# Optimization experiments

Hardware: AMD Instinct MI355X
Metric: run time of the kernel (lower is better)

The kernel has to match this reference:

```python
import jax, jax.numpy as jnp
from jax import lax
import numpy as np

B, H, W = 16, 512, 512
NBINS = 256
MARGIN_EYE = 12
BLUR_SIZE = 5
ALPHA_SKIN, ALPHA_EYE, ALPHA_LIP = 0.3, 0.8, 0.1


def de_norm(x):
    return jnp.clip((x + 1.0) * 0.5, 0.0, 1.0)


def renorm(x):
    return x * 2.0 - 1.0


def _match_channel(src, ref, w_s, w_r):
    # src/ref: (P,) pixel values in [0,255]; w_s/w_r: (P,) mask weights
    b_s = jnp.clip(src.astype(jnp.int32), 0, NBINS - 1)
    b_r = jnp.clip(ref.astype(jnp.int32), 0, NBINS - 1)
    h_s = jnp.zeros((NBINS,), src.dtype).at[b_s].add(w_s)   # masked histogram
    h_r = jnp.zeros((NBINS,), ref.dtype).at[b_r].add(w_r)
    cdf_s = jnp.cumsum(h_s) / jnp.maximum(jnp.sum(h_s), 1e-6)
    cdf_r = jnp.cumsum(h_r) / jnp.maximum(jnp.sum(h_r), 1e-6)
    # CDF-matching transfer table (equiv. of cal_trans in PSGAN/EleGANt)
    table = jnp.clip(jnp.searchsorted(cdf_r, cdf_s), 0, NBINS - 1).astype(src.dtype)
    return table[b_s]


def masked_his_match(image_s, image_r, mask_s, mask_r):
    # image: (3,H,W), mask: (1,H,W)
    s = de_norm(image_s) * 255.0 * mask_s
    r = de_norm(image_r) * 255.0 * mask_r
    w_s = mask_s.reshape(-1)
    w_r = mask_r.reshape(-1)
    matched = jax.vmap(_match_channel, in_axes=(0, 0, None, None))(
        s.reshape(3, -1), r.reshape(3, -1), w_s, w_r).reshape(s.shape)
    matched = jnp.where(mask_s > 0, matched, s)  # only masked pixels replaced
    return renorm(matched / 255.0)


def expand_area(mask, margin):
    # morphological dilation (max pool) of (1,H,W) mask
    k = 2 * margin + 1
    return lax.reduce_window(mask, 0.0, lax.max, (1, k, k), (1, 1, 1), 'SAME')


def mask_blur(mask, blur_size):
    # box blur; 'valid' mode: blurred support kept inside original mask
    k = blur_size
    s = lax.reduce_window(mask, 0.0, lax.add, (1, k, k), (1, 1, 1), 'SAME') / float(k * k)
    return s * mask


def generate_pgt(image_s, image_r, mask_s, mask_r, lms_s, lms_r):
    pgt = image_s
    # skin (channel 1)
    m = mask_s[1:2]
    pgt = (1.0 - m) * pgt + m * masked_his_match(image_s, image_r, m, mask_r[1:2])
    # neck (channel 4)
    m = mask_s[4:5]
    pgt = (1.0 - m) * pgt + m * masked_his_match(image_s, image_r, m, mask_r[4:5])
    # lip (channel 0)
    m = mask_s[0:1]
    pgt = (1.0 - m) * pgt + m * masked_his_match(image_s, image_r, m, mask_r[0:1])
    # eyes (channels 2,3), dilated and intersected with skin
    m_se = expand_area(jnp.sum(mask_s[2:4], axis=0, keepdims=True), MARGIN_EYE) * mask_s[1:2]
    m_re = expand_area(jnp.sum(mask_r[2:4], axis=0, keepdims=True), MARGIN_EYE) * mask_r[1:2]
    eye_match = masked_his_match(image_s, image_r, m_se, m_re)
    mb = mask_blur(m_se, BLUR_SIZE)
    pgt = (1.0 - mb) * pgt + mb * eye_match
    # fine_align (reconstructed, simplified: per-region alpha blend of reference,
    # landmark warp omitted -- helper source not provided)
    for m, a in ((mask_s[1:2], ALPHA_SKIN), (m_se, ALPHA_EYE), (mask_s[0:1], ALPHA_LIP)):
        pgt = (1.0 - a * m) * pgt + (a * m) * image_r
    return pgt


def setup_inputs() -> dict:
    key = jax.random.key(0)
    ks = jax.random.split(key, 6)
    sources = jax.random.uniform(ks[0], (B, 3, H, W), jnp.float32, -1.0, 1.0)
    targets = jax.random.uniform(ks[1], (B, 3, H, W), jnp.float32, -1.0, 1.0)
    mask_srcs = (jax.random.uniform(ks[2], (B, 5, H, W)) < 0.3).astype(jnp.float32)
    mask_tars = (jax.random.uniform(ks[3], (B, 5, H, W)) < 0.3).astype(jnp.float32)
    lms_srcs = jax.random.uniform(ks[4], (B, 68, 2), jnp.float32, 0.0, float(H))
    lms_tars = jax.random.uniform(ks[5], (B, 68, 2), jnp.float32, 0.0, float(H))
    return {"sources": sources, "targets": targets, "mask_srcs": mask_srcs,
            "mask_tars": mask_tars, "lms_srcs": lms_srcs, "lms_tars": lms_tars}


def reference(sources, targets, mask_srcs, mask_tars, lms_srcs, lms_tars):
    # vmap over batch replaces the per-sample Python loop of ComposePGT.forward
    return jax.vmap(generate_pgt)(sources, targets, mask_srcs, mask_tars, lms_srcs, lms_tars)
```

## Files before the change

### kernel.cpp

```cpp
#include <hip/hip_runtime.h>
#include <stdint.h>

#define BB 16
#define HH 512
#define WW 512
#define HW (HH*WW)
#define NB 256


__device__ __forceinline__ float denorm255(float x) {
    return fminf(fmaxf((x + 1.0f) * 0.5f, 0.0f), 1.0f) * 255.0f;
}
__device__ __forceinline__ float renorm_lut(int t) {
    return ((float)t / 255.0f) * 2.0f - 1.0f;
}
__device__ __forceinline__ uint32_t alignb(uint32_t hi, uint32_t lo, int r) {
    return (uint32_t)(((((uint64_t)hi) << 32) | lo) >> (8 * r));
}

__global__ void __launch_bounds__(256) prep_kernel(
    const float* __restrict__ ms, const float* __restrict__ mr,
    uint32_t* __restrict__ C)
{
    int t = blockIdx.x * 256 + threadIdx.x;
    const int perSide = BB * (HW / 4);
    int side = t / perSide;
    int rem  = t - side * perSide;
    int b    = rem / (HW / 4);
    int c    = rem - b * (HW / 4);
    const float* base = (side == 0 ? ms : mr) + (size_t)b * 5 * HW;
    float4 m0 = ((const float4*)(base + 0 * (size_t)HW))[c];
    float4 m1 = ((const float4*)(base + 1 * (size_t)HW))[c];
    float4 m2 = ((const float4*)(base + 2 * (size_t)HW))[c];
    float4 m3 = ((const float4*)(base + 3 * (size_t)HW))[c];
    float4 m4 = ((const float4*)(base + 4 * (size_t)HW))[c];
    float a0[4] = {m0.x, m0.y, m0.z, m0.w};
    float a1[4] = {m1.x, m1.y, m1.z, m1.w};
    float a2[4] = {m2.x, m2.y, m2.z, m2.w};
    float a3[4] = {m3.x, m3.y, m3.z, m3.w};
    float a4[4] = {m4.x, m4.y, m4.z, m4.w};
    uint32_t w = 0;
    #pragma unroll
    for (int j = 0; j < 4; j++) {
        uint32_t e  = (uint32_t)(a2[j] + a3[j]);
        uint32_t pb = (a0[j] > 0.f ? 4u : 0u) | (a1[j] > 0.f ? 8u : 0u)
                    | (a4[j] > 0.f ? 16u : 0u);
        w |= (e | pb) << (8 * j);
    }
    C[t] = w;
}

__global__ void __launch_bounds__(256) hor_kernel(
    const uint32_t* __restrict__ C, uint32_t* __restrict__ eh)
{
    int t   = blockIdx.x * 256 + threadIdx.x;
    int row = t >> 7;
    int w   = t & 127;
    const uint32_t* rp = C + (size_t)row * 128;
    uint32_t arr[7];
    #pragma unroll
    for (int k = 0; k < 7; k++) {
        int idx = w + k - 3;
        arr[k] = (idx >= 0 && idx < 128) ? (rp[idx] & 0x03030303u) : 0u;
    }
    uint32_t acc = arr[3];
    #pragma unroll
    for (int s = 1; s <= 12; s++) {
        int a = s >> 2, r = s & 3;
        uint32_t vp, vm;
        if (r == 0) {
            vp = arr[3 + a];
            vm = arr[3 - a];
        } else {
            vp = alignb(arr[3 + a + 1], arr[3 + a], r);
            int am = (s + 3) >> 2;
            vm = alignb(arr[3 - am + 1], arr[3 - am], 4 - r);
        }
        acc |= vp | vm;
    }
    eh[t] = acc;
}

__global__ void __launch_bounds__(256) ver_kernel(
    const uint32_t* __restrict__ eh, uint32_t* __restrict__ C)
{
    int t   = blockIdx.x * 256 + threadIdx.x;
    int sb  = t >> 12;
    int rem = t & 4095;
    int yg  = rem >> 5;
    int ck  = rem & 31;
    int y0  = yg << 2;
    const uint4* P = (const uint4*)(eh + (size_t)sb * (HW / 4));
    auto R = [&](int y) -> uint4 {
        uint4 z = {0, 0, 0, 0};
        if (y < 0 || y >= HH) return z;
        return P[y * 32 + ck];
    };
    uint4 core = {0, 0, 0, 0};
    #pragma unroll
    for (int yy = -9; yy <= 12; yy++) {
        uint4 r = R(y0 + yy);
        core.x |= r.x; core.y |= r.y; core.z |= r.z; core.w |= r.w;
    }
    uint4 b0 = R(y0 - 12), b1 = R(y0 - 11), b2 = R(y0 - 10);
    uint4 a0 = R(y0 + 13), a1 = R(y0 + 14), a2 = R(y0 + 15);

    uint4* C4 = (uint4*)(C + (size_t)sb * (HW / 4));
    #pragma unroll
    for (int i = 0; i < 4; i++) {
        uint4 v = core;
        if (i == 0) { v.x|=b0.x|b1.x|b2.x; v.y|=b0.y|b1.y|b2.y; v.z|=b0.z|b1.z|b2.z; v.w|=b0.w|b1.w|b2.w; }
        if (i == 1) { v.x|=b1.x|b2.x|a0.x; v.y|=b1.y|b2.y|a0.y; v.z|=b1.z|b2.z|a0.z; v.w|=b1.w|b2.w|a0.w; }
        if (i == 2) { v.x|=b2.x|a0.x|a1.x; v.y|=b2.y|a0.y|a1.y; v.z|=b2.z|a0.z|a1.z; v.w|=b2.w|a0.w|a1.w; }
        if (i == 3) { v.x|=a0.x|a1.x|a2.x; v.y|=a0.y|a1.y|a2.y; v.z|=a0.z|a1.z|a2.z; v.w|=a0.w|a1.w|a2.w; }
        int idx = (y0 + i) * 32 + ck;
        uint4 cw = C4[idx];
        #pragma unroll
        for (int q = 0; q < 4; q++) {
            uint32_t vv = (&v.x)[q];
            uint32_t cc = (&cw.x)[q];
            uint32_t t3 = vv & (vv >> 1) & 0x01010101u;
            vv -= t3;
            uint32_t m1b = (cc >> 3) & 0x01010101u;
            vv &= m1b * 255u;
            (&cw.x)[q] = cc | (vv << 5);
        }
        C4[idx] = cw;
    }
}

__global__ void __launch_bounds__(256) blur_kernel(
    const uint32_t* __restrict__ C, uint32_t* __restrict__ mbs)
{
    int t   = blockIdx.x * 256 + threadIdx.x;
    int b   = t >> 14;
    b = t >> 16;
    int rem = t & 65535;
    int y   = rem >> 7;
    int w   = rem & 127;
    const uint32_t* P = C + (size_t)b * (HW / 4);
    uint32_t vm1 = 0, v0 = 0, vp1 = 0;
    #pragma unroll
    for (int dy = -2; dy <= 2; dy++) {
        int yy = y + dy;
        if (yy < 0 || yy >= HH) continue;
        const uint32_t* rp = P + yy * 128;
        if (w > 0)   vm1 += (rp[w - 1] >> 5) & 0x03030303u;
        v0 += (rp[w] >> 5) & 0x03030303u;
        if (w < 127) vp1 += (rp[w + 1] >> 5) & 0x03030303u;
    }
    uint32_t s = v0;
    s += alignb(v0, vm1, 2);
    s += alignb(v0, vm1, 3);
    s += alignb(vp1, v0, 1);
    s += alignb(vp1, v0, 2);
    mbs[t] = s;
}

#define HB 64
__global__ void __launch_bounds__(256) hist_kernel(
    const float* __restrict__ src, const float* __restrict__ tgt,
    const uint32_t* __restrict__ C, int* __restrict__ hist)
{
    int bs  = blockIdx.x / HB;
    int blk = blockIdx.x % HB;
    int b = bs >> 1, side = bs & 1;
    const float* img = (side ? tgt : src) + (size_t)b * 3 * HW;
    const float4* i0 = (const float4*)(img);
    const float4* i1 = (const float4*)(img + HW);
    const float4* i2 = (const float4*)(img + 2 * (size_t)HW);
    const uint32_t* pc = C + (size_t)(side * BB + b) * (HW / 4);

    __shared__ int h[12 * NB];
    for (int i = threadIdx.x; i < 12 * NB; i += 256) h[i] = 0;
    __syncthreads();

    for (int c = blk * 256 + threadIdx.x; c < HW / 4; c += HB * 256) {
        float4 v0 = i0[c], v1 = i1[c], v2 = i2[c];
        uint32_t cw = pc[c];
        float d0[4] = {denorm255(v0.x), denorm255(v0.y), denorm255(v0.z), denorm255(v0.w)};
        float d1[4] = {denorm255(v1.x), denorm255(v1.y), denorm255(v1.z), denorm255(v1.w)};
        float d2[4] = {denorm255(v2.x), denorm255(v2.y), denorm255(v2.z), denorm255(v2.w)};
        #pragma unroll
        for (int j = 0; j < 4; j++) {
            uint32_t pb = (cw >> (8 * j)) & 0xFFu;
            if (pb & 8u) {
                atomicAdd(&h[0 * NB + min((int)d0[j], 255)], 1);
                atomicAdd(&h[1 * NB + min((int)d1[j], 255)], 1);
                atomicAdd(&h[2 * NB + min((int)d2[j], 255)], 1);
            }
            if (pb & 16u) {
                atomicAdd(&h[3 * NB + min((int)d0[j], 255)], 1);
                atomicAdd(&h[4 * NB + min((int)d1[j], 255)], 1);
                atomicAdd(&h[5 * NB + min((int)d2[j], 255)], 1);
            }
            if (pb & 4u) {
                atomicAdd(&h[6 * NB + min((int)d0[j], 255)], 1);
                atomicAdd(&h[7 * NB + min((int)d1[j], 255)], 1);
                atomicAdd(&h[8 * NB + min((int)d2[j], 255)], 1);
            }
            int mei = (int)((pb >> 5) & 3u);
            if (mei) {
                float fm = (float)mei;
                atomicAdd(&h[ 9 * NB + min((int)(d0[j] * fm), 255)], mei);
                atomicAdd(&h[10 * NB + min((int)(d1[j] * fm), 255)], mei);
                atomicAdd(&h[11 * NB + min((int)(d2[j] * fm), 255)], mei);
            }
        }
    }
    __syncthreads();
    int* gh = hist + (size_t)bs * 12 * NB;
    for (int i = threadIdx.x; i < 12 * NB; i += 256)
        if (h[i]) atomicAdd(&gh[i], h[i]);
}

__global__ void __launch_bounds__(NB) table_kernel(
    const int* __restrict__ hist, uint8_t* __restrict__ table)
{
    int idx = blockIdx.x;
    int c = idx % 3; int rest = idx / 3; int rg = rest & 3; int b = rest >> 2;
    const int* hs = hist + ((size_t)((b * 2 + 0) * 4 + rg) * 3 + c) * NB;
    const int* hr = hist + ((size_t)((b * 2 + 1) * 4 + rg) * 3 + c) * NB;
    __shared__ int a[NB];
    __shared__ float cr[NB];
    int t = threadIdx.x;

    a[t] = hs[t];
    __syncthreads();
    for (int off = 1; off < NB; off <<= 1) {
        int v = (t >= off) ? a[t - off] : 0;
        __syncthreads();
        a[t] += v;
        __syncthreads();
    }
    int totS = a[NB - 1];
    int cumS = a[t];
    __syncthreads();

    a[t] = hr[t];
    __syncthreads();
    for (int off = 1; off < NB; off <<= 1) {
        int v = (t >= off) ? a[t - off] : 0;
        __syncthreads();
        a[t] += v;
        __syncthreads();
    }
    int totR = a[NB - 1];
    cr[t] = (float)a[t] / fmaxf((float)totR, 1e-6f);
    float v = (float)cumS / fmaxf((float)totS, 1e-6f);
    __syncthreads();

    int cnt = 0;
    for (int j = 0; j < NB; j++) cnt += (cr[j] < v) ? 1 : 0;
    table[(size_t)idx * NB + t] = (uint8_t)min(cnt, 255);
}

#define CB 64
__global__ void __launch_bounds__(256) compose_kernel(
    const float* __restrict__ src, const float* __restrict__ tgt,
    const uint32_t* __restrict__ C, const uint32_t* __restrict__ mbs,
    const uint8_t* __restrict__ table, float* __restrict__ out)
{
    int b   = blockIdx.x / CB;
    int blk = blockIdx.x % CB;
    __shared__ uint8_t tb[12 * NB];
    const uint8_t* gt = table + (size_t)b * 12 * NB;
    for (int i = threadIdx.x; i < 12 * NB; i += 256) tb[i] = gt[i];
    __syncthreads();

    const float4* s0 = (const float4*)(src + (size_t)b * 3 * HW);
    const float4* s1 = s0 + HW / 4;
    const float4* s2 = s1 + HW / 4;
    const float4* t0 = (const float4*)(tgt + (size_t)b * 3 * HW);
    const float4* t1 = t0 + HW / 4;
    const float4* t2 = t1 + HW / 4;
    const uint32_t* pc = C + (size_t)b * (HW / 4);
    const uint32_t* qc = mbs + (size_t)b * (HW / 4);
    float4* o0 = (float4*)(out + (size_t)b * 3 * HW);
    float4* o1 = o0 + HW / 4;
    float4* o2 = o1 + HW / 4;

    for (int c = blk * 256 + threadIdx.x; c < HW / 4; c += CB * 256) {
        float4 x0 = s0[c], x1 = s1[c], x2 = s2[c];
        float4 r0 = t0[c], r1 = t1[c], r2 = t2[c];
        uint32_t cw = pc[c];
        uint32_t qw = qc[c];
        float X0[4] = {x0.x, x0.y, x0.z, x0.w};
        float X1[4] = {x1.x, x1.y, x1.z, x1.w};
        float X2[4] = {x2.x, x2.y, x2.z, x2.w};
        float R0[4] = {r0.x, r0.y, r0.z, r0.w};
        float R1[4] = {r1.x, r1.y, r1.z, r1.w};
        float R2[4] = {r2.x, r2.y, r2.z, r2.w};
        float O0[4], O1[4], O2[4];
        #pragma unroll
        for (int j = 0; j < 4; j++) {
            uint32_t pb = (cw >> (8 * j)) & 0xFFu;
            float q = (float)((qw >> (8 * j)) & 0xFFu);
            float m0f = (float)((pb >> 2) & 1u);
            float m1f = (float)((pb >> 3) & 1u);
            float m4f = (float)((pb >> 4) & 1u);
            float fm  = (float)((pb >> 5) & 3u);
            float d0 = denorm255(X0[j]), d1 = denorm255(X1[j]), d2 = denorm255(X2[j]);
            float p0 = X0[j], p1 = X1[j], p2 = X2[j];
            {
                float e0 = renorm_lut(tb[0 * NB + min((int)(d0 * m1f), 255)]);
                float e1 = renorm_lut(tb[1 * NB + min((int)(d1 * m1f), 255)]);
                float e2 = renorm_lut(tb[2 * NB + min((int)(d2 * m1f), 255)]);
                p0 = (1.0f - m1f) * p0 + m1f * e0;
                p1 = (1.0f - m1f) * p1 + m1f * e1;
                p2 = (1.0f - m1f) * p2 + m1f * e2;
            }
            {
                float e0 = renorm_lut(tb[3 * NB + min((int)(d0 * m4f), 255)]);
                float e1 = renorm_lut(tb[4 * NB + min((int)(d1 * m4f), 255)]);
                float e2 = renorm_lut(tb[5 * NB + min((int)(d2 * m4f), 255)]);
                p0 = (1.0f - m4f) * p0 + m4f * e0;
                p1 = (1.0f - m4f) * p1 + m4f * e1;
                p2 = (1.0f - m4f) * p2 + m4f * e2;
            }
            {
                float e0 = renorm_lut(tb[6 * NB + min((int)(d0 * m0f), 255)]);
                float e1 = renorm_lut(tb[7 * NB + min((int)(d1 * m0f), 255)]);
                float e2 = renorm_lut(tb[8 * NB + min((int)(d2 * m0f), 255)]);
                p0 = (1.0f - m0f) * p0 + m0f * e0;
                p1 = (1.0f - m0f) * p1 + m0f * e1;
                p2 = (1.0f - m0f) * p2 + m0f * e2;
            }
            {
                float mb = (q * (1.0f / 25.0f)) * fm;
                float e0 = renorm_lut(tb[ 9 * NB + min((int)(d0 * fm), 255)]);
                float e1 = renorm_lut(tb[10 * NB + min((int)(d1 * fm), 255)]);
                float e2 = renorm_lut(tb[11 * NB + min((int)(d2 * fm), 255)]);
                p0 = (1.0f - mb) * p0 + mb * e0;
                p1 = (1.0f - mb) * p1 + mb * e1;
                p2 = (1.0f - mb) * p2 + mb * e2;
            }
            float a = 0.3f * m1f;
            p0 = (1.0f - a) * p0 + a * R0[j];
            p1 = (1.0f - a) * p1 + a * R1[j];
            p2 = (1.0f - a) * p2 + a * R2[j];
            a = 0.8f * fm;
            p0 = (1.0f - a) * p0 + a * R0[j];
            p1 = (1.0f - a) * p1 + a * R1[j];
            p2 = (1.0f - a) * p2 + a * R2[j];
            a = 0.1f * m0f;
            p0 = (1.0f - a) * p0 + a * R0[j];
            p1 = (1.0f - a) * p1 + a * R1[j];
            p2 = (1.0f - a) * p2 + a * R2[j];
            O0[j] = p0; O1[j] = p1; O2[j] = p2;
        }
        float4 w0 = {O0[0], O0[1], O0[2], O0[3]};
        float4 w1 = {O1[0], O1[1], O1[2], O1[3]};
        float4 w2 = {O2[0], O2[1], O2[2], O2[3]};
        o0[c] = w0; o1[c] = w1; o2[c] = w2;
    }
}

extern "C" void kernel_launch(void* const* d_in, const int* in_sizes, int n_in,
                              void* d_out, int out_size, void* d_ws, size_t ws_size,
                              hipStream_t stream) {
    const float* src = (const float*)d_in[0];
    const float* tgt = (const float*)d_in[1];
    const float* ms  = (const float*)d_in[2];
    const float* mr  = (const float*)d_in[3];
    float* out = (float*)d_out;

    uint8_t* ws = (uint8_t*)d_ws;
    uint32_t* C   = (uint32_t*)(ws);
    uint32_t* eh  = (uint32_t*)(ws + (size_t)2 * BB * HW);
    uint32_t* mbs = (uint32_t*)(ws + (size_t)4 * BB * HW);
    int* hist     = (int*)(ws + (size_t)5 * BB * HW);
    uint8_t* table = ws + (size_t)5 * BB * HW + (size_t)2 * BB * 12 * NB * 4;

    hipMemsetAsync(hist, 0, (size_t)2 * BB * 12 * NB * sizeof(int), stream);

    prep_kernel<<<2 * BB * HW / 4 / 256, 256, 0, stream>>>(ms, mr, C);
    hor_kernel<<<2 * BB * HW / 4 / 256, 256, 0, stream>>>(C, eh);
    ver_kernel<<<2 * BB * (HH / 4) * (WW / 16) / 256, 256, 0, stream>>>(eh, C);
    blur_kernel<<<BB * HW / 4 / 256, 256, 0, stream>>>(C, mbs);
    hist_kernel<<<2 * BB * HB, 256, 0, stream>>>(src, tgt, C, hist);
    table_kernel<<<BB * 4 * 3, NB, 0, stream>>>(hist, table);
    compose_kernel<<<BB * CB, 256, 0, stream>>>(src, tgt, C, mbs, table, out);
}
```

Baseline: 343.1 us.

## Fuse mask prep with horizontal dilation and widen per-thread work in blur, hist, compose

Mask packing and horizontal dilation now run in one kernel that shares the row through LDS, so the intermediate packed mask is no longer re-read from global memory by a separate pass. Blur now handles 16 pixels per thread with uint4 loads. The histogram kernel processes 8 pixels per iteration with half as many blocks. Compose drops its grid-stride loop for one thread per 8 pixels, which means many more blocks each reloading the 3 KB LUT into shared memory. That extra per-block LUT load is the main added cost.

```diff
diff --git a/kernel.cpp b/kernel.cpp
--- a/kernel.cpp
+++ b/kernel.cpp
@@ -18,67 +18,85 @@
     return (uint32_t)(((((uint64_t)hi) << 32) | lo) >> (8 * r));
 }
 
-__global__ void __launch_bounds__(256) prep_kernel(
+__global__ void __launch_bounds__(256) prep_hor_kernel(
     const float* __restrict__ ms, const float* __restrict__ mr,
-    uint32_t* __restrict__ C)
-{
-    int t = blockIdx.x * 256 + threadIdx.x;
-    const int perSide = BB * (HW / 4);
-    int side = t / perSide;
-    int rem  = t - side * perSide;
-    int b    = rem / (HW / 4);
-    int c    = rem - b * (HW / 4);
-    const float* base = (side == 0 ? ms : mr) + (size_t)b * 5 * HW;
-    float4 m0 = ((const float4*)(base + 0 * (size_t)HW))[c];
-    float4 m1 = ((const float4*)(base + 1 * (size_t)HW))[c];
-    float4 m2 = ((const float4*)(base + 2 * (size_t)HW))[c];
-    float4 m3 = ((const float4*)(base + 3 * (size_t)HW))[c];
-    float4 m4 = ((const float4*)(base + 4 * (size_t)HW))[c];
-    float a0[4] = {m0.x, m0.y, m0.z, m0.w};
-    float a1[4] = {m1.x, m1.y, m1.z, m1.w};
-    float a2[4] = {m2.x, m2.y, m2.z, m2.w};
-    float a3[4] = {m3.x, m3.y, m3.z, m3.w};
-    float a4[4] = {m4.x, m4.y, m4.z, m4.w};
-    uint32_t w = 0;
-    #pragma unroll
-    for (int j = 0; j < 4; j++) {
-        uint32_t e  = (uint32_t)(a2[j] + a3[j]);
-        uint32_t pb = (a0[j] > 0.f ? 4u : 0u) | (a1[j] > 0.f ? 8u : 0u)
-                    | (a4[j] > 0.f ? 16u : 0u);
-        w |= (e | pb) << (8 * j);
-    }
-    C[t] = w;
-}
-
-__global__ void __launch_bounds__(256) hor_kernel(
-    const uint32_t* __restrict__ C, uint32_t* __restrict__ eh)
-{
-    int t   = blockIdx.x * 256 + threadIdx.x;
-    int row = t >> 7;
-    int w   = t & 127;
-    const uint32_t* rp = C + (size_t)row * 128;
-    uint32_t arr[7];
-    #pragma unroll
-    for (int k = 0; k < 7; k++) {
-        int idx = w + k - 3;
-        arr[k] = (idx >= 0 && idx < 128) ? (rp[idx] & 0x03030303u) : 0u;
-    }
-    uint32_t acc = arr[3];
-    #pragma unroll
-    for (int s = 1; s <= 12; s++) {
-        int a = s >> 2, r = s & 3;
-        uint32_t vp, vm;
-        if (r == 0) {
-            vp = arr[3 + a];
-            vm = arr[3 - a];
-        } else {
-            vp = alignb(arr[3 + a + 1], arr[3 + a], r);
-            int am = (s + 3) >> 2;
-            vm = alignb(arr[3 - am + 1], arr[3 - am], 4 - r);
-        }
-        acc |= vp | vm;
-    }
-    eh[t] = acc;
+    uint4* __restrict__ C, uint4* __restrict__ eh)
+{
+    int blk  = blockIdx.x;
+    int side = blk >> 10;
+    int rem  = blk & 1023;
+    int b    = rem >> 6;
+    int rg   = rem & 63;
+    int r    = threadIdx.x >> 5;
+    int c    = threadIdx.x & 31;
+    int y    = (rg << 3) + r;
+
+    const float* base = (side ? mr : ms) + (size_t)b * 5 * HW + (size_t)y * WW + c * 16;
+
+    float4 v[5][4];
+    #pragma unroll
+    for (int p = 0; p < 5; p++) {
+        const float4* pp = (const float4*)(base + (size_t)p * HW);
+        #pragma unroll
+        for (int q = 0; q < 4; q++) v[p][q] = pp[q];
+    }
+    uint4 cw, ew;
+    #pragma unroll
+    for (int w = 0; w < 4; w++) {
+        uint32_t wc = 0;
+        #pragma unroll
+        for (int j = 0; j < 4; j++) {
+            float a0 = (&v[0][w].x)[j];
+            float a1 = (&v[1][w].x)[j];
+            float a2 = (&v[2][w].x)[j];
+            float a3 = (&v[3][w].x)[j];
+            float a4 = (&v[4][w].x)[j];
+            uint32_t e  = (uint32_t)(a2 + a3);
+            uint32_t pb = (a0 > 0.f ? 4u : 0u) | (a1 > 0.f ? 8u : 0u)
+                        | (a4 > 0.f ? 16u : 0u);
+            wc |= (e | pb) << (8 * j);
+        }
+        (&cw.x)[w] = wc;
+        (&ew.x)[w] = wc & 0x03030303u;
+    }
+    size_t plane = (size_t)(side * BB + b);
+    int widx = y * 32 + c;
+    C[plane * (HW / 16) + widx] = cw;
+
+    __shared__ uint4 se[8][32];
+    se[r][c] = ew;
+    __syncthreads();
+
+    const uint4 zero4 = {0u, 0u, 0u, 0u};
+    uint4 L = (c > 0)  ? se[r][c - 1] : zero4;
+    uint4 M = se[r][c];
+    uint4 R = (c < 31) ? se[r][c + 1] : zero4;
+    uint32_t W[12] = {L.x, L.y, L.z, L.w, M.x, M.y, M.z, M.w, R.x, R.y, R.z, R.w};
+
+    uint4 outw;
+    #pragma unroll
+    for (int k = 0; k < 4; k++) {
+        uint32_t arr[7];
+        #pragma unroll
+        for (int i = 0; i < 7; i++) arr[i] = W[k + 1 + i];
+        uint32_t acc = arr[3];
+        #pragma unroll
+        for (int s = 1; s <= 12; s++) {
+            int a = s >> 2, rr = s & 3;
+            uint32_t vp, vm;
+            if (rr == 0) {
+                vp = arr[3 + a];
+                vm = arr[3 - a];
+            } else {
+                vp = alignb(arr[3 + a + 1], arr[3 + a], rr);
+                int am = (s + 3) >> 2;
+                vm = alignb(arr[3 - am + 1], arr[3 - am], 4 - rr);
+            }
+            acc |= vp | vm;
+        }
+        (&outw.x)[k] = acc;
+    }
+    eh[plane * (HW / 16) + widx] = outw;
 }
 
 __global__ void __launch_bounds__(256) ver_kernel(
@@ -130,34 +148,79 @@
 }
 
 __global__ void __launch_bounds__(256) blur_kernel(
-    const uint32_t* __restrict__ C, uint32_t* __restrict__ mbs)
-{
-    int t   = blockIdx.x * 256 + threadIdx.x;
-    int b   = t >> 14;
-    b = t >> 16;
-    int rem = t & 65535;
-    int y   = rem >> 7;
-    int w   = rem & 127;
+    const uint32_t* __restrict__ C, uint4* __restrict__ mbs)
+{
+    int t = blockIdx.x * 256 + threadIdx.x;
+    int b = t >> 14;
+    int rem = t & 16383;
+    int y = rem >> 5;
+    int c = rem & 31;
     const uint32_t* P = C + (size_t)b * (HW / 4);
-    uint32_t vm1 = 0, v0 = 0, vp1 = 0;
+    int c4 = c << 2;
+    uint32_t s[6] = {0u, 0u, 0u, 0u, 0u, 0u};
     #pragma unroll
     for (int dy = -2; dy <= 2; dy++) {
         int yy = y + dy;
         if (yy < 0 || yy >= HH) continue;
         const uint32_t* rp = P + yy * 128;
-        if (w > 0)   vm1 += (rp[w - 1] >> 5) & 0x03030303u;
-        v0 += (rp[w] >> 5) & 0x03030303u;
-        if (w < 127) vp1 += (rp[w + 1] >> 5) & 0x03030303u;
-    }
-    uint32_t s = v0;
-    s += alignb(v0, vm1, 2);
-    s += alignb(v0, vm1, 3);
-    s += alignb(vp1, v0, 1);
-    s += alignb(vp1, v0, 2);
-    mbs[t] = s;
-}
-
-#define HB 64
+        uint32_t l = (c > 0)  ? rp[c4 - 1] : 0u;
+        uint4 m = *((const uint4*)(rp + c4));
+        uint32_t rr = (c < 31) ? rp[c4 + 4] : 0u;
+        s[0] += (l   >> 5) & 0x03030303u;
+        s[1] += (m.x >> 5) & 0x03030303u;
+        s[2] += (m.y >> 5) & 0x03030303u;
+        s[3] += (m.z >> 5) & 0x03030303u;
+        s[4] += (m.w >> 5) & 0x03030303u;
+        s[5] += (rr  >> 5) & 0x03030303u;
+    }
+    uint4 o;
+    #pragma unroll
+    for (int k = 0; k < 4; k++) {
+        uint32_t v = s[k + 1];
+        v += alignb(s[k + 1], s[k],     2);
+        v += alignb(s[k + 1], s[k],     3);
+        v += alignb(s[k + 2], s[k + 1], 1);
+        v += alignb(s[k + 2], s[k + 1], 2);
+        (&o.x)[k] = v;
+    }
+    mbs[t] = o;
+}
+
+#define HB 32
+__device__ __forceinline__ void hist4(int* h, uint32_t cw,
+                                      float4 v0, float4 v1, float4 v2)
+{
+    float d0[4] = {denorm255(v0.x), denorm255(v0.y), denorm255(v0.z), denorm255(v0.w)};
+    float d1[4] = {denorm255(v1.x), denorm255(v1.y), denorm255(v1.z), denorm255(v1.w)};
+    float d2[4] = {denorm255(v2.x), denorm255(v2.y), denorm255(v2.z), denorm255(v2.w)};
+    #pragma unroll
+    for (int j = 0; j < 4; j++) {
+        uint32_t pb = (cw >> (8 * j)) & 0xFFu;
+        if (pb & 8u) {
+            atomicAdd(&h[0 * NB + min((int)d0[j], 255)], 1);
+            atomicAdd(&h[1 * NB + min((int)d1[j], 255)], 1);
+            atomicAdd(&h[2 * NB + min((int)d2[j], 255)], 1);
+        }
+        if (pb & 16u) {
+            atomicAdd(&h[3 * NB + min((int)d0[j], 255)], 1);
+            atomicAdd(&h[4 * NB + min((int)d1[j], 255)], 1);
+            atomicAdd(&h[5 * NB + min((int)d2[j], 255)], 1);
+        }
+        if (pb & 4u) {
+            atomicAdd(&h[6 * NB + min((int)d0[j], 255)], 1);
+            atomicAdd(&h[7 * NB + min((int)d1[j], 255)], 1);
+            atomicAdd(&h[8 * NB + min((int)d2[j], 255)], 1);
+        }
+        int mei = (int)((pb >> 5) & 3u);
+        if (mei) {
+            float fm = (float)mei;
+            atomicAdd(&h[ 9 * NB + min((int)(d0[j] * fm), 255)], mei);
+            atomicAdd(&h[10 * NB + min((int)(d1[j] * fm), 255)], mei);
+            atomicAdd(&h[11 * NB + min((int)(d2[j] * fm), 255)], mei);
+        }
+    }
+}
+
 __global__ void __launch_bounds__(256) hist_kernel(
     const float* __restrict__ src, const float* __restrict__ tgt,
     const uint32_t* __restrict__ C, int* __restrict__ hist)
@@ -169,44 +232,19 @@
     const float4* i0 = (const float4*)(img);
     const float4* i1 = (const float4*)(img + HW);
     const float4* i2 = (const float4*)(img + 2 * (size_t)HW);
-    const uint32_t* pc = C + (size_t)(side * BB + b) * (HW / 4);
+    const uint2* pc = (const uint2*)(C + (size_t)(side * BB + b) * (HW / 4));
 
     __shared__ int h[12 * NB];
     for (int i = threadIdx.x; i < 12 * NB; i += 256) h[i] = 0;
     __syncthreads();
 
-    for (int c = blk * 256 + threadIdx.x; c < HW / 4; c += HB * 256) {
-        float4 v0 = i0[c], v1 = i1[c], v2 = i2[c];
-        uint32_t cw = pc[c];
-        float d0[4] = {denorm255(v0.x), denorm255(v0.y), denorm255(v0.z), denorm255(v0.w)};
-        float d1[4] = {denorm255(v1.x), denorm255(v1.y), denorm255(v1.z), denorm255(v1.w)};
-        float d2[4] = {denorm255(v2.x), denorm255(v2.y), denorm255(v2.z), denorm255(v2.w)};
-        #pragma unroll
-        for (int j = 0; j < 4; j++) {
-            uint32_t pb = (cw >> (8 * j)) & 0xFFu;
-            if (pb & 8u) {
-                atomicAdd(&h[0 * NB + min((int)d0[j], 255)], 1);
-                atomicAdd(&h[1 * NB + min((int)d1[j], 255)], 1);
-                atomicAdd(&h[2 * NB + min((int)d2[j], 255)], 1);
-            }
-            if (pb & 16u) {
-                atomicAdd(&h[3 * NB + min((int)d0[j], 255)], 1);
-                atomicAdd(&h[4 * NB + min((int)d1[j], 255)], 1);
-                atomicAdd(&h[5 * NB + min((int)d2[j], 255)], 1);
-            }
-            if (pb & 4u) {
-                atomicAdd(&h[6 * NB + min((int)d0[j], 255)], 1);
-                atomicAdd(&h[7 * NB + min((int)d1[j], 255)], 1);
-                atomicAdd(&h[8 * NB + min((int)d2[j], 255)], 1);
-            }
-            int mei = (int)((pb >> 5) & 3u);
-            if (mei) {
-                float fm = (float)mei;
-                atomicAdd(&h[ 9 * NB + min((int)(d0[j] * fm), 255)], mei);
-                atomicAdd(&h[10 * NB + min((int)(d1[j] * fm), 255)], mei);
-                atomicAdd(&h[11 * NB + min((int)(d2[j] * fm), 255)], mei);
-            }
-        }
+    for (int c = blk * 256 + threadIdx.x; c < HW / 8; c += HB * 256) {
+        uint2 cw = pc[c];
+        float4 a0 = i0[2 * c], b0 = i0[2 * c + 1];
+        float4 a1 = i1[2 * c], b1 = i1[2 * c + 1];
+        float4 a2 = i2[2 * c], b2 = i2[2 * c + 1];
+        hist4(h, cw.x, a0, a1, a2);
+        hist4(h, cw.y, b0, b1, b2);
     }
     __syncthreads();
     int* gh = hist + (size_t)bs * 12 * NB;
@@ -255,17 +293,90 @@
     table[(size_t)idx * NB + t] = (uint8_t)min(cnt, 255);
 }
 
-#define CB 64
+__device__ __forceinline__ void proc4(uint32_t cw, uint32_t qw,
+    float4 x0, float4 x1, float4 x2, float4 r0, float4 r1, float4 r2,
+    const uint8_t* tb, float4& o0, float4& o1, float4& o2)
+{
+    float X0[4] = {x0.x, x0.y, x0.z, x0.w};
+    float X1[4] = {x1.x, x1.y, x1.z, x1.w};
+    float X2[4] = {x2.x, x2.y, x2.z, x2.w};
+    float R0[4] = {r0.x, r0.y, r0.z, r0.w};
+    float R1[4] = {r1.x, r1.y, r1.z, r1.w};
+    float R2[4] = {r2.x, r2.y, r2.z, r2.w};
+    #pragma unroll
+    for (int j = 0; j < 4; j++) {
+        uint32_t pb = (cw >> (8 * j)) & 0xFFu;
+        float q = (float)((qw >> (8 * j)) & 0xFFu);
+        float m0f = (float)((pb >> 2) & 1u);
+        float m1f = (float)((pb >> 3) & 1u);
+        float m4f = (float)((pb >> 4) & 1u);
+        float fm  = (float)((pb >> 5) & 3u);
+        float d0 = denorm255(X0[j]), d1 = denorm255(X1[j]), d2 = denorm255(X2[j]);
+        float p0 = X0[j], p1 = X1[j], p2 = X2[j];
+        {
+            float e0 = renorm_lut(tb[0 * NB + min((int)(d0 * m1f), 255)]);
+            float e1 = renorm_lut(tb[1 * NB + min((int)(d1 * m1f), 255)]);
+            float e2 = renorm_lut(tb[2 * NB + min((int)(d2 * m1f), 255)]);
+            p0 = (1.0f - m1f) * p0 + m1f * e0;
+            p1 = (1.0f - m1f) * p1 + m1f * e1;
+            p2 = (1.0f - m1f) * p2 + m1f * e2;
+        }
+        {
+            float e0 = renorm_lut(tb[3 * NB + min((int)(d0 * m4f), 255)]);
+            float e1 = renorm_lut(tb[4 * NB + min((int)(d1 * m4f), 255)]);
+            float e2 = renorm_lut(tb[5 * NB + min((int)(d2 * m4f), 255)]);
+            p0 = (1.0f - m4f) * p0 + m4f * e0;
+            p1 = (1.0f - m4f) * p1 + m4f * e1;
+            p2 = (1.0f - m4f) * p2 + m4f * e2;
+        }
+        {
+            float e0 = renorm_lut(tb[6 * NB + min((int)(d0 * m0f), 255)]);
+            float e1 = renorm_lut(tb[7 * NB + min((int)(d1 * m0f), 255)]);
+            float e2 = renorm_lut(tb[8 * NB + min((int)(d2 * m0f), 255)]);
+            p0 = (1.0f - m0f) * p0 + m0f * e0;
+            p1 = (1.0f - m0f) * p1 + m0f * e1;
+            p2 = (1.0f - m0f) * p2 + m0f * e2;
+        }
+        {
+            float mb = (q * (1.0f / 25.0f)) * fm;
+            float e0 = renorm_lut(tb[ 9 * NB + min((int)(d0 * fm), 255)]);
+            float e1 = renorm_lut(tb[10 * NB + min((int)(d1 * fm), 255)]);
+            float e2 = renorm_lut(tb[11 * NB + min((int)(d2 * fm), 255)]);
+            p0 = (1.0f - mb) * p0 + mb * e0;
+            p1 = (1.0f - mb) * p1 + mb * e1;
+            p2 = (1.0f - mb) * p2 + mb * e2;
+        }
+        float a = 0.3f * m1f;
+        p0 = (1.0f - a) * p0 + a * R0[j];
+        p1 = (1.0f - a) * p1 + a * R1[j];
+        p2 = (1.0f - a) * p2 + a * R2[j];
+        a = 0.8f * fm;
+        p0 = (1.0f - a) * p0 + a * R0[j];
+        p1 = (1.0f - a) * p1 + a * R1[j];
+        p2 = (1.0f - a) * p2 + a * R2[j];
+        a = 0.1f * m0f;
+        p0 = (1.0f - a) * p0 + a * R0[j];
+        p1 = (1.0f - a) * p1 + a * R1[j];
+        p2 = (1.0f - a) * p2 + a * R2[j];
+        (&o0.x)[j] = p0; (&o1.x)[j] = p1; (&o2.x)[j] = p2;
+    }
+}
+
 __global__ void __launch_bounds__(256) compose_kernel(
     const float* __restrict__ src, const float* __restrict__ tgt,
     const uint32_t* __restrict__ C, const uint32_t* __restrict__ mbs,
     const uint8_t* __restrict__ table, float* __restrict__ out)
 {
-    int b   = blockIdx.x / CB;
-    int blk = blockIdx.x % CB;
+    int t = blockIdx.x * 256 + threadIdx.x;
+    int b = t >> 15;
+    int c = t & 32767;
+
     __shared__ uint8_t tb[12 * NB];
-    const uint8_t* gt = table + (size_t)b * 12 * NB;
-    for (int i = threadIdx.x; i < 12 * NB; i += 256) tb[i] = gt[i];
+    {
+        const uint32_t* gt = (const uint32_t*)(table + (size_t)b * 12 * NB);
+        uint32_t* tw = (uint32_t*)tb;
+        for (int i = threadIdx.x; i < 12 * NB / 4; i += 256) tw[i] = gt[i];
+    }
     __syncthreads();
 
     const float4* s0 = (const float4*)(src + (size_t)b * 3 * HW);
@@ -274,86 +385,28 @@
     const float4* t0 = (const float4*)(tgt + (size_t)b * 3 * HW);
     const float4* t1 = t0 + HW / 4;
     const float4* t2 = t1 + HW / 4;
-    const uint32_t* pc = C + (size_t)b * (HW / 4);
-    const uint32_t* qc = mbs + (size_t)b * (HW / 4);
+    const uint2* pc = (const uint2*)(C + (size_t)b * (HW / 4));
+    const uint2* qc = (const uint2*)(mbs + (size_t)b * (HW / 4));
     float4* o0 = (float4*)(out + (size_t)b * 3 * HW);
     float4* o1 = o0 + HW / 4;
     float4* o2 = o1 + HW / 4;
 
-    for (int c = blk * 256 + threadIdx.x; c < HW / 4; c += CB * 256) {
-        float4 x0 = s0[c], x1 = s1[c], x2 = s2[c];
-        float4 r0 = t0[c], r1 = t1[c], r2 = t2[c];
-        uint32_t cw = pc[c];
-        uint32_t qw = qc[c];
-        float X0[4] = {x0.x, x0.y, x0.z, x0.w};
-        float X1[4] = {x1.x, x1.y, x1.z, x1.w};
-        float X2[4] = {x2.x, x2.y, x2.z, x2.w};
-        float R0[4] = {r0.x, r0.y, r0.z, r0.w};
-        float R1[4] = {r1.x, r1.y, r1.z, r1.w};
-        float R2[4] = {r2.x, r2.y, r2.z, r2.w};
-        float O0[4], O1[4], O2[4];
-        #pragma unroll
-        for (int j = 0; j < 4; j++) {
-            uint32_t pb = (cw >> (8 * j)) & 0xFFu;
-            float q = (float)((qw >> (8 * j)) & 0xFFu);
-            float m0f = (float)((pb >> 2) & 1u);
-            float m1f = (float)((pb >> 3) & 1u);
-            float m4f = (float)((pb >> 4) & 1u);
-            float fm  = (float)((pb >> 5) & 3u);
-            float d0 = denorm255(X0[j]), d1 = denorm255(X1[j]), d2 = denorm255(X2[j]);
-            float p0 = X0[j], p1 = X1[j], p2 = X2[j];
-            {
-                float e0 = renorm_lut(tb[0 * NB + min((int)(d0 * m1f), 255)]);
-                float e1 = renorm_lut(tb[1 * NB + min((int)(d1 * m1f), 255)]);
-                float e2 = renorm_lut(tb[2 * NB + min((int)(d2 * m1f), 255)]);
-                p0 = (1.0f - m1f) * p0 + m1f * e0;
-                p1 = (1.0f - m1f) * p1 + m1f * e1;
-                p2 = (1.0f - m1f) * p2 + m1f * e2;
-            }
-            {
-                float e0 = renorm_lut(tb[3 * NB + min((int)(d0 * m4f), 255)]);
-                float e1 = renorm_lut(tb[4 * NB + min((int)(d1 * m4f), 255)]);
-                float e2 = renorm_lut(tb[5 * NB + min((int)(d2 * m4f), 255)]);
-                p0 = (1.0f - m4f) * p0 + m4f * e0;
-                p1 = (1.0f - m4f) * p1 + m4f * e1;
-                p2 = (1.0f - m4f) * p2 + m4f * e2;
-            }
-            {
-                float e0 = renorm_lut(tb[6 * NB + min((int)(d0 * m0f), 255)]);
-                float e1 = renorm_lut(tb[7 * NB + min((int)(d1 * m0f), 255)]);
-                float e2 = renorm_lut(tb[8 * NB + min((int)(d2 * m0f), 255)]);
-                p0 = (1.0f - m0f) * p0 + m0f * e0;
-                p1 = (1.0f - m0f) * p1 + m0f * e1;
-                p2 = (1.0f - m0f) * p2 + m0f * e2;
-            }
-            {
-                float mb = (q * (1.0f / 25.0f)) * fm;
-                float e0 = renorm_lut(tb[ 9 * NB + min((int)(d0 * fm), 255)]);
-                float e1 = renorm_lut(tb[10 * NB + min((int)(d1 * fm), 255)]);
-                float e2 = renorm_lut(tb[11 * NB + min((int)(d2 * fm), 255)]);
-                p0 = (1.0f - mb) * p0 + mb * e0;
-                p1 = (1.0f - mb) * p1 + mb * e1;
-                p2 = (1.0f - mb) * p2 + mb * e2;
-            }
-            float a = 0.3f * m1f;
-            p0 = (1.0f - a) * p0 + a * R0[j];
-            p1 = (1.0f - a) * p1 + a * R1[j];
-            p2 = (1.0f - a) * p2 + a * R2[j];
-            a = 0.8f * fm;
-            p0 = (1.0f - a) * p0 + a * R0[j];
-            p1 = (1.0f - a) * p1 + a * R1[j];
-            p2 = (1.0f - a) * p2 + a * R2[j];
-            a = 0.1f * m0f;
-            p0 = (1.0f - a) * p0 + a * R0[j];
-            p1 = (1.0f - a) * p1 + a * R1[j];
-            p2 = (1.0f - a) * p2 + a * R2[j];
-            O0[j] = p0; O1[j] = p1; O2[j] = p2;
-        }
-        float4 w0 = {O0[0], O0[1], O0[2], O0[3]};
-        float4 w1 = {O1[0], O1[1], O1[2], O1[3]};
-        float4 w2 = {O2[0], O2[1], O2[2], O2[3]};
-        o0[c] = w0; o1[c] = w1; o2[c] = w2;
-    }
+    uint2 cw = pc[c];
+    uint2 qw = qc[c];
+    float4 xa0 = s0[2 * c], xb0 = s0[2 * c + 1];
+    float4 xa1 = s1[2 * c], xb1 = s1[2 * c + 1];
+    float4 xa2 = s2[2 * c], xb2 = s2[2 * c + 1];
+    float4 ra0 = t0[2 * c], rb0 = t0[2 * c + 1];
+    float4 ra1 = t1[2 * c], rb1 = t1[2 * c + 1];
+    float4 ra2 = t2[2 * c], rb2 = t2[2 * c + 1];
+
+    float4 oa0, oa1, oa2, ob0, ob1, ob2;
+    proc4(cw.x, qw.x, xa0, xa1, xa2, ra0, ra1, ra2, tb, oa0, oa1, oa2);
+    proc4(cw.y, qw.y, xb0, xb1, xb2, rb0, rb1, rb2, tb, ob0, ob1, ob2);
+
+    o0[2 * c] = oa0; o0[2 * c + 1] = ob0;
+    o1[2 * c] = oa1; o1[2 * c + 1] = ob1;
+    o2[2 * c] = oa2; o2[2 * c + 1] = ob2;
 }
 
 extern "C" void kernel_launch(void* const* d_in, const int* in_sizes, int n_in,
@@ -374,11 +427,10 @@
 
     hipMemsetAsync(hist, 0, (size_t)2 * BB * 12 * NB * sizeof(int), stream);
 
-    prep_kernel<<<2 * BB * HW / 4 / 256, 256, 0, stream>>>(ms, mr, C);
-    hor_kernel<<<2 * BB * HW / 4 / 256, 256, 0, stream>>>(C, eh);
+    prep_hor_kernel<<<2 * BB * 64, 256, 0, stream>>>(ms, mr, (uint4*)C, (uint4*)eh);
     ver_kernel<<<2 * BB * (HH / 4) * (WW / 16) / 256, 256, 0, stream>>>(eh, C);
-    blur_kernel<<<BB * HW / 4 / 256, 256, 0, stream>>>(C, mbs);
+    blur_kernel<<<BB * (HW / 16) / 256, 256, 0, stream>>>(C, (uint4*)mbs);
     hist_kernel<<<2 * BB * HB, 256, 0, stream>>>(src, tgt, C, hist);
     table_kernel<<<BB * 4 * 3, NB, 0, stream>>>(hist, table);
-    compose_kernel<<<BB * CB, 256, 0, stream>>>(src, tgt, C, mbs, table, out);
-}
+    compose_kernel<<<BB * (HW / 8) / 256, 256, 0, stream>>>(src, tgt, C, mbs, table, out);
+}
```

After: 333.7 us. -2.7%, faster.
